# Kernel optimization log

Hardware: AMD Instinct MI355X
Metric: run time of the kernel (lower is better)

The kernel has to match this reference:

```python
import jax, jax.numpy as jnp
import numpy as np

N, M, D = 8192, 8192, 64
_LIM = 36.0

def _softplus(x):
    # LogexpTransformation.inverse_transform: x if x > 36 else log1p(exp(x))
    return jnp.where(x > _LIM, x, jnp.log1p(jnp.exp(jnp.minimum(x, _LIM))))

def setup_inputs() -> dict:
    key = jax.random.key(0)
    k1, k2, k3 = jax.random.split(key, 3)
    X = jax.random.normal(k1, (N, D), dtype=jnp.float32)
    Z = jax.random.normal(k2, (M, D), dtype=jnp.float32)
    l_raw = jax.random.uniform(k3, (D,), dtype=jnp.float32)
    sigma_f_raw = jnp.ones((), dtype=jnp.float32)
    return {"X": X, "Z": Z, "l_raw": l_raw, "sigma_f_raw": sigma_f_raw}

def reference(X, Z, l_raw, sigma_f_raw):
    l = _softplus(l_raw)                     # [D] length scales
    sigma_f = _softplus(sigma_f_raw)         # scalar signal variance
    inv_length = 1.0 / (l * l)               # [D]
    w = jnp.sqrt(inv_length)                 # scale features instead of [N,M,D] broadcast
    Xs = X * w                               # [N,D]
    Zs = Z * w                               # [M,D]
    # sum_d inv_length[d]*(X-Z)^2 = |Xs|^2 + |Zs|^2 - 2 Xs.Zs  (GEMM-expansion)
    x2 = jnp.sum(Xs * Xs, axis=1)            # [N]
    z2 = jnp.sum(Zs * Zs, axis=1)            # [M]
    cross = Xs @ Zs.T                        # [N,M]
    dist = x2[:, None] + z2[None, :] - 2.0 * cross
    return sigma_f * jnp.exp(-0.5 * dist)
```

## Files before the change

kernel.cpp:

```cpp
#include <hip/hip_runtime.h>
#include <hip/hip_bf16.h>
#include <math.h>

#define NROWS 8192
#define MCOLS 8192
#define DK    64
#define TILE_G 8

typedef _Float16 f16x8 __attribute__((ext_vector_type(8)));
typedef __attribute__((ext_vector_type(8))) short bf16x8;
typedef __attribute__((ext_vector_type(4))) float f32x4;

#define WS_XH 0u
#define WS_ZH (1u << 20)
#define WS_HX (2u << 20)
#define WS_HZ ((2u << 20) + 32768u)
#define WS_NEED ((size_t)(2u << 20) + 65536u)

#define SQRT_L2E 1.2011224087864498f

__device__ __forceinline__ float softplus_f(float x) {
    return x > 36.0f ? x : log1pf(expf(fminf(x, 36.0f)));
}

__global__ void rbf_prep(const float* __restrict__ X, const float* __restrict__ Z,
                         const float* __restrict__ lraw, const float* __restrict__ sraw,
                         char* __restrict__ ws) {
    __shared__ float wsc[DK];
    if (threadIdx.x < DK)
        wsc[threadIdx.x] = SQRT_L2E / softplus_f(lraw[threadIdx.x]);
    __syncthreads();

    int tid = blockIdx.x * 256 + threadIdx.x;
    bool isZ = tid >= 65536;
    int t = tid & 65535;
    int row = t >> 3;
    int kc = t & 7;
    const float* src = (isZ ? Z : X) + (size_t)row * DK + kc * 8;
    float4 v0 = *(const float4*)(src);
    float4 v1 = *(const float4*)(src + 4);
    float f[8] = {v0.x, v0.y, v0.z, v0.w, v1.x, v1.y, v1.z, v1.w};
    f16x8 hv;
    float sq = 0.0f;
    #pragma unroll
    for (int j = 0; j < 8; ++j) {
        _Float16 h = (_Float16)(f[j] * wsc[kc * 8 + j]);
        hv[j] = h;
        float hf = (float)h;
        sq += hf * hf;
    }
    sq += __shfl_xor(sq, 1);
    sq += __shfl_xor(sq, 2);
    sq += __shfl_xor(sq, 4);
    *(f16x8*)(ws + (isZ ? WS_ZH : WS_XH) + (size_t)row * 128 + kc * 16) = hv;
    if (kc == 0) {
        float* nrm = (float*)(ws + (isZ ? WS_HZ : WS_HX));
        float v = 0.5f * sq;
        if (isZ) v -= log2f(softplus_f(sraw[0]));
        nrm[row] = v;
    }
}

__launch_bounds__(512, 4)
__global__ void rbf_main(const char* __restrict__ ws, float* __restrict__ out) {
    __shared__ __align__(16) char smem[49152];

    int bid = blockIdx.x;
    int s = (bid & 7) * 64 + (bid >> 3);
    int tR = s >> 3;
    int cg = s & 7;

    const int tid  = threadIdx.x;
    const int lane = tid & 63;
    const int wid  = tid >> 6;
    const int wr = wid >> 1, wc = wid & 1;
    const int lr = lane & 15, lg = lane >> 4;
    const int swz = (lr & 7) << 4;

    const int o0 = tid * 16, o1 = tid * 16 + 8192;
    const int r0 = o0 >> 7, cb0 = o0 & 127;
    const int r1 = o1 >> 7, cb1 = o1 & 127;
    const int d0 = r0 * 128 + (cb0 ^ ((r0 & 7) << 4));
    const int d1 = r1 * 128 + (cb1 ^ ((r1 & 7) << 4));

    {
        const char* xsrc = ws + WS_XH + (size_t)tR * 16384;
        *(float4*)(smem + d0) = *(const float4*)(xsrc + o0);
        *(float4*)(smem + d1) = *(const float4*)(xsrc + o1);
        const char* zsrc = ws + WS_ZH + (size_t)(cg * TILE_G) * 16384;
        *(float4*)(smem + 16384 + d0) = *(const float4*)(zsrc + o0);
        *(float4*)(smem + 16384 + d1) = *(const float4*)(zsrc + o1);
    }
    __syncthreads();

    f16x8 xf[2][2];
    #pragma unroll
    for (int ks = 0; ks < 2; ++ks)
        #pragma unroll
        for (int mi = 0; mi < 2; ++mi)
            xf[ks][mi] = *(const f16x8*)(smem + (wr * 32 + mi * 16 + lr) * 128
                                         + ((lg * 16 + ks * 64) ^ swz));

    const float* hx = (const float*)(ws + WS_HX);
    const float* hz = (const float*)(ws + WS_HZ);
    float4 hxa[2];
    #pragma unroll
    for (int mi = 0; mi < 2; ++mi)
        hxa[mi] = *(const float4*)(hx + tR * 128 + wr * 32 + mi * 16 + lg * 4);

    for (int g = 0; g < TILE_G; ++g) {
        const int cur = g & 1;
        const int tC = cg * TILE_G + g;

        float4 z0, z1;
        if (g + 1 < TILE_G) {
            const char* zsrc = ws + WS_ZH + (size_t)(tC + 1) * 16384;
            z0 = *(const float4*)(zsrc + o0);
            z1 = *(const float4*)(zsrc + o1);
        }

        const char* zb = smem + 16384 + cur * 16384;
        f32x4 acc[2][4];
        #pragma unroll
        for (int a = 0; a < 2; ++a)
            #pragma unroll
            for (int b = 0; b < 4; ++b) acc[a][b] = f32x4{0.f, 0.f, 0.f, 0.f};
        #pragma unroll
        for (int ks = 0; ks < 2; ++ks) {
            const int kb = ((lg * 16 + ks * 64) ^ swz);
            f16x8 bfr[4];
            #pragma unroll
            for (int ni = 0; ni < 4; ++ni)
                bfr[ni] = *(const f16x8*)(zb + (wc * 64 + ni * 16 + lr) * 128 + kb);
            #pragma unroll
            for (int mi = 0; mi < 2; ++mi)
                #pragma unroll
                for (int ni = 0; ni < 4; ++ni)
                    acc[mi][ni] = __builtin_amdgcn_mfma_f32_16x16x32_f16(
                        xf[ks][mi], bfr[ni], acc[mi][ni], 0, 0, 0);
        }

        float hzv[4];
        #pragma unroll
        for (int ni = 0; ni < 4; ++ni)
            hzv[ni] = hz[tC * 128 + wc * 64 + ni * 16 + lr];
        #pragma unroll
        for (int mi = 0; mi < 2; ++mi) {
            int grow0 = tR * 128 + wr * 32 + mi * 16 + lg * 4;
            #pragma unroll
            for (int ni = 0; ni < 4; ++ni) {
                int gcol = tC * 128 + wc * 64 + ni * 16 + lr;
                size_t obase = (size_t)grow0 * MCOLS + gcol;
                #pragma unroll
                for (int j = 0; j < 4; ++j) {
                    float arg = acc[mi][ni][j] - hxa[mi][j] - hzv[ni];
                    out[obase + (size_t)j * MCOLS] = __builtin_amdgcn_exp2f(arg);
                }
            }
        }

        if (g + 1 < TILE_G) {
            char* zn = smem + 16384 + (1 - cur) * 16384;
            *(float4*)(zn + d0) = z0;
            *(float4*)(zn + d1) = z1;
            __syncthreads();
        }
    }
}

__launch_bounds__(512, 4)
__global__ void rbf_fused(const float* __restrict__ X, const float* __restrict__ Z,
                          const float* __restrict__ lraw, const float* __restrict__ sraw,
                          float* __restrict__ out) {
    __shared__ __align__(16) char smem[65536];
    __shared__ float hxz[256];
    __shared__ float wsc[DK];
    __shared__ float sigf_s;

    const int tid = threadIdx.x;
    const int tR = blockIdx.y;
    const int tC = blockIdx.x;

    if (tid < DK) wsc[tid] = 1.0f / softplus_f(lraw[tid]);
    if (tid == 511) sigf_s = softplus_f(sraw[0]);
    __syncthreads();

    #pragma unroll
    for (int i = 0; i < 4; ++i) {
        int rfull = i * 64 + (tid >> 3);
        int r = rfull & 127;
        int kc = tid & 7;
        bool isB = rfull >= 128;
        const float* src = isB ? (Z + (size_t)(tC * 128 + r) * DK + kc * 8)
                               : (X + (size_t)(tR * 128 + r) * DK + kc * 8);
        float4 v0 = *(const float4*)(src);
        float4 v1 = *(const float4*)(src + 4);
        float f[8] = {v0.x, v0.y, v0.z, v0.w, v1.x, v1.y, v1.z, v1.w};
        bf16x8 hv, lv;
        float sq = 0.0f;
        #pragma unroll
        for (int j = 0; j < 8; ++j) {
            float fv = f[j] * wsc[kc * 8 + j];
            sq += fv * fv;
            unsigned int u = __float_as_uint(fv);
            u += 0x7fffu + ((u >> 16) & 1u);
            unsigned short h = (unsigned short)(u >> 16);
            hv[j] = (short)h;
            float hf = __uint_as_float(((unsigned int)h) << 16);
            unsigned int u2 = __float_as_uint(fv - hf);
            u2 += 0x7fffu + ((u2 >> 16) & 1u);
            lv[j] = (short)(unsigned short)(u2 >> 16);
        }
        sq += __shfl_xor(sq, 1);
        sq += __shfl_xor(sq, 2);
        sq += __shfl_xor(sq, 4);
        if (kc == 0) hxz[rfull] = 0.5f * sq;
        int halfOff = isB ? 32768 : 0;
        int byteOff = r * 128 + ((kc * 16) ^ ((r & 7) << 4));
        *(bf16x8*)(smem + halfOff + byteOff) = hv;
        *(bf16x8*)(smem + halfOff + 16384 + byteOff) = lv;
    }
    __syncthreads();

    const int lane = tid & 63;
    const int wid  = tid >> 6;
    const int wr = wid >> 1;
    const int wc = wid & 1;
    const int lr = lane & 15;
    const int lg = lane >> 4;
    const int swz = (lr & 7) << 4;

    f32x4 acc[2][4];
    #pragma unroll
    for (int a = 0; a < 2; ++a)
        #pragma unroll
        for (int b = 0; b < 4; ++b) acc[a][b] = f32x4{0.f, 0.f, 0.f, 0.f};

    #pragma unroll
    for (int pass = 0; pass < 3; ++pass) {
        const char* Ap = smem + ((pass == 2) ? 16384 : 0);
        const char* Bp = smem + 32768 + ((pass == 1) ? 16384 : 0);
        #pragma unroll
        for (int ks = 0; ks < 2; ++ks) {
            int kb = ((lg * 16 + ks * 64) ^ swz);
            bf16x8 af[2], bfr[4];
            #pragma unroll
            for (int mi = 0; mi < 2; ++mi)
                af[mi] = *(const bf16x8*)(Ap + (wr * 32 + mi * 16 + lr) * 128 + kb);
            #pragma unroll
            for (int ni = 0; ni < 4; ++ni)
                bfr[ni] = *(const bf16x8*)(Bp + (wc * 64 + ni * 16 + lr) * 128 + kb);
            #pragma unroll
            for (int mi = 0; mi < 2; ++mi)
                #pragma unroll
                for (int ni = 0; ni < 4; ++ni)
                    acc[mi][ni] = __builtin_amdgcn_mfma_f32_16x16x32_bf16(
                        af[mi], bfr[ni], acc[mi][ni], 0, 0, 0);
        }
    }

    const float sf = sigf_s;
    #pragma unroll
    for (int mi = 0; mi < 2; ++mi) {
        int row0 = wr * 32 + mi * 16 + lg * 4;
        #pragma unroll
        for (int ni = 0; ni < 4; ++ni) {
            int col = wc * 64 + ni * 16 + lr;
            float hzv = hxz[128 + col];
            size_t obase = (size_t)(tR * 128 + row0) * MCOLS + (size_t)(tC * 128 + col);
            #pragma unroll
            for (int j = 0; j < 4; ++j) {
                float arg = acc[mi][ni][j] - (hxz[row0 + j] + hzv);
                out[obase + (size_t)j * MCOLS] = sf * __expf(arg);
            }
        }
    }
}

extern "C" void kernel_launch(void* const* d_in, const int* in_sizes, int n_in,
                              void* d_out, int out_size, void* d_ws, size_t ws_size,
                              hipStream_t stream) {
    const float* X = (const float*)d_in[0];
    const float* Z = (const float*)d_in[1];
    const float* l = (const float*)d_in[2];
    const float* s = (const float*)d_in[3];
    float* out = (float*)d_out;
    if (ws_size >= WS_NEED && d_ws != nullptr) {
        char* ws = (char*)d_ws;
        rbf_prep<<<512, 256, 0, stream>>>(X, Z, l, s, ws);
        rbf_main<<<512, 512, 0, stream>>>(ws, out);
    } else {
        dim3 grid(MCOLS / 128, NROWS / 128);
        rbf_fused<<<grid, dim3(512), 0, stream>>>(X, Z, l, s, out);
    }
}
```

Baseline: 53.37 us.

## Store prep operands in MFMA fragment order and load them directly from global

The prep kernel now writes the scaled fp16 X and Z rows in a fragment-major layout that matches the MFMA lane mapping. The main kernel then loads A and B fragments straight from global memory (L2) with one contiguous 16-byte load per lane, and drops the LDS staging, swizzle, double buffering and per-tile barriers. This removes LDS traffic and synchronisation. In exchange, the Z fragments are re-read from global or L2 by each wave with no prefetch overlap, and all wave pairs sharing a column re-read the same data.

```diff
diff --git a/kernel.cpp b/kernel.cpp
--- a/kernel.cpp
+++ b/kernel.cpp
@@ -52,7 +52,13 @@
     sq += __shfl_xor(sq, 1);
     sq += __shfl_xor(sq, 2);
     sq += __shfl_xor(sq, 4);
-    *(f16x8*)(ws + (isZ ? WS_ZH : WS_XH) + (size_t)row * 128 + kc * 16) = hv;
+    {
+        int c  = row >> 4;
+        int ks = kc >> 2;
+        int lif = (row & 15) | ((kc & 3) << 4);
+        *(f16x8*)(ws + (isZ ? WS_ZH : WS_XH)
+                  + ((size_t)((c * 2 + ks) * 64 + lif) << 4)) = hv;
+    }
     if (kc == 0) {
         float* nrm = (float*)(ws + (isZ ? WS_HZ : WS_HX));
         float v = 0.5f * sq;
@@ -63,8 +69,6 @@
 
 __launch_bounds__(512, 4)
 __global__ void rbf_main(const char* __restrict__ ws, float* __restrict__ out) {
-    __shared__ __align__(16) char smem[49152];
-
     int bid = blockIdx.x;
     int s = (bid & 7) * 64 + (bid >> 3);
     int tR = s >> 3;
@@ -75,70 +79,51 @@
     const int wid  = tid >> 6;
     const int wr = wid >> 1, wc = wid & 1;
     const int lr = lane & 15, lg = lane >> 4;
-    const int swz = (lr & 7) << 4;
-
-    const int o0 = tid * 16, o1 = tid * 16 + 8192;
-    const int r0 = o0 >> 7, cb0 = o0 & 127;
-    const int r1 = o1 >> 7, cb1 = o1 & 127;
-    const int d0 = r0 * 128 + (cb0 ^ ((r0 & 7) << 4));
-    const int d1 = r1 * 128 + (cb1 ^ ((r1 & 7) << 4));
-
-    {
-        const char* xsrc = ws + WS_XH + (size_t)tR * 16384;
-        *(float4*)(smem + d0) = *(const float4*)(xsrc + o0);
-        *(float4*)(smem + d1) = *(const float4*)(xsrc + o1);
-        const char* zsrc = ws + WS_ZH + (size_t)(cg * TILE_G) * 16384;
-        *(float4*)(smem + 16384 + d0) = *(const float4*)(zsrc + o0);
-        *(float4*)(smem + 16384 + d1) = *(const float4*)(zsrc + o1);
-    }
-    __syncthreads();
-
-    f16x8 xf[2][2];
-    #pragma unroll
-    for (int ks = 0; ks < 2; ++ks)
-        #pragma unroll
-        for (int mi = 0; mi < 2; ++mi)
-            xf[ks][mi] = *(const f16x8*)(smem + (wr * 32 + mi * 16 + lr) * 128
-                                         + ((lg * 16 + ks * 64) ^ swz));
-
+
+    const char* Xf = ws + WS_XH;
+    const char* Zf = ws + WS_ZH;
     const float* hx = (const float*)(ws + WS_HX);
     const float* hz = (const float*)(ws + WS_HZ);
+
+    f16x8 af[2][2];
+    #pragma unroll
+    for (int ks = 0; ks < 2; ++ks)
+        #pragma unroll
+        for (int mi = 0; mi < 2; ++mi) {
+            int cx = tR * 8 + wr * 2 + mi;
+            af[ks][mi] = *(const f16x8*)(Xf + ((size_t)((cx * 2 + ks) * 64 + lane) << 4));
+        }
+
     float4 hxa[2];
     #pragma unroll
     for (int mi = 0; mi < 2; ++mi)
         hxa[mi] = *(const float4*)(hx + tR * 128 + wr * 32 + mi * 16 + lg * 4);
 
     for (int g = 0; g < TILE_G; ++g) {
-        const int cur = g & 1;
         const int tC = cg * TILE_G + g;
 
-        float4 z0, z1;
-        if (g + 1 < TILE_G) {
-            const char* zsrc = ws + WS_ZH + (size_t)(tC + 1) * 16384;
-            z0 = *(const float4*)(zsrc + o0);
-            z1 = *(const float4*)(zsrc + o1);
-        }
-
-        const char* zb = smem + 16384 + cur * 16384;
+        f16x8 bfr[2][4];
+        #pragma unroll
+        for (int ks = 0; ks < 2; ++ks)
+            #pragma unroll
+            for (int ni = 0; ni < 4; ++ni) {
+                int cz = tC * 8 + wc * 4 + ni;
+                bfr[ks][ni] = *(const f16x8*)(Zf + ((size_t)((cz * 2 + ks) * 64 + lane) << 4));
+            }
+
         f32x4 acc[2][4];
         #pragma unroll
         for (int a = 0; a < 2; ++a)
             #pragma unroll
             for (int b = 0; b < 4; ++b) acc[a][b] = f32x4{0.f, 0.f, 0.f, 0.f};
         #pragma unroll
-        for (int ks = 0; ks < 2; ++ks) {
-            const int kb = ((lg * 16 + ks * 64) ^ swz);
-            f16x8 bfr[4];
-            #pragma unroll
-            for (int ni = 0; ni < 4; ++ni)
-                bfr[ni] = *(const f16x8*)(zb + (wc * 64 + ni * 16 + lr) * 128 + kb);
+        for (int ks = 0; ks < 2; ++ks)
             #pragma unroll
             for (int mi = 0; mi < 2; ++mi)
                 #pragma unroll
                 for (int ni = 0; ni < 4; ++ni)
                     acc[mi][ni] = __builtin_amdgcn_mfma_f32_16x16x32_f16(
-                        xf[ks][mi], bfr[ni], acc[mi][ni], 0, 0, 0);
-        }
+                        af[ks][mi], bfr[ks][ni], acc[mi][ni], 0, 0, 0);
 
         float hzv[4];
         #pragma unroll
@@ -157,13 +142,6 @@
                     out[obase + (size_t)j * MCOLS] = __builtin_amdgcn_exp2f(arg);
                 }
             }
-        }
-
-        if (g + 1 < TILE_G) {
-            char* zn = smem + 16384 + (1 - cur) * 16384;
-            *(float4*)(zn + d0) = z0;
-            *(float4*)(zn + d1) = z1;
-            __syncthreads();
         }
     }
 }
```

Measured after the change: 56.31 us. +5.5%, slower.
